# Kernel tuning notes

Hardware: AMD Instinct MI355X
Metric: run time of the kernel (lower is better)

Reference implementation:

```python
import jax, jax.numpy as jnp
import numpy as np

N_NODES = 50000
N_EDGES = 800000
DIM_IN = 64
DIM_H = 32
HEADS = 4
NUM_CLASSES = 10
NEG_SLOPE = 0.2  # DGL GATv2Conv default negative_slope


def _gatv2_layer(x, W_src, b_src, W_dst, b_dst, attn, src, dst):
    """DGL GATv2Conv (share_weights=False, eval mode so feat_drop is identity).
    x: [N, F_in]; attn: [H, D]; returns [N, H, D]."""
    N = x.shape[0]
    H, D = attn.shape
    fs = (x @ W_src + b_src).reshape(N, H, D)  # source projection
    fd = (x @ W_dst + b_dst).reshape(N, H, D)  # destination projection
    # per-edge additive attention: leaky_relu(fs[u] + fd[v]) . attn  -> [E, H]
    e = jax.nn.leaky_relu(fs[src] + fd[dst], NEG_SLOPE)  # [E, H, D]
    s = jnp.einsum('ehd,hd->eh', e, attn)  # [E, H]
    # edge softmax over incoming edges of each destination node
    smax = jax.lax.stop_gradient(
        jax.ops.segment_max(s, dst, num_segments=N))  # [N, H]
    es = jnp.exp(s - smax[dst])
    denom = jax.ops.segment_sum(es, dst, num_segments=N)  # [N, H]
    alpha = es / denom[dst]
    # weighted scatter-aggregate of source features
    out = jax.ops.segment_sum(alpha[:, :, None] * fs[src], dst, num_segments=N)
    return out  # [N, H, D]


def setup_inputs() -> dict:
    key = jax.random.key(0)
    ks = jax.random.split(key, 16)
    sc = 0.05
    inp = {
        'g_feats': jax.random.normal(ks[0], (N_NODES, DIM_IN), jnp.float32),
        'edge_src': jax.random.randint(ks[1], (N_EDGES,), 0, N_NODES, jnp.int32),
        'edge_dst': jax.random.randint(ks[2], (N_EDGES,), 0, N_NODES, jnp.int32),
        # input embedding Linear(dim_in, dim_h)
        'W_in': jax.random.normal(ks[3], (DIM_IN, DIM_H), jnp.float32) * sc,
        'b_in': jnp.zeros((DIM_H,), jnp.float32),
        # GATv2 layer 1: Linear(dim_h, heads*dim_h) for src/dst + attn [H, D]
        'W1_src': jax.random.normal(ks[4], (DIM_H, HEADS * DIM_H), jnp.float32) * sc,
        'b1_src': jnp.zeros((HEADS * DIM_H,), jnp.float32),
        'W1_dst': jax.random.normal(ks[5], (DIM_H, HEADS * DIM_H), jnp.float32) * sc,
        'b1_dst': jnp.zeros((HEADS * DIM_H,), jnp.float32),
        'attn1': jax.random.normal(ks[6], (HEADS, DIM_H), jnp.float32) * sc,
        # GATv2 layer 2
        'W2_src': jax.random.normal(ks[7], (DIM_H, HEADS * DIM_H), jnp.float32) * sc,
        'b2_src': jnp.zeros((HEADS * DIM_H,), jnp.float32),
        'W2_dst': jax.random.normal(ks[8], (DIM_H, HEADS * DIM_H), jnp.float32) * sc,
        'b2_dst': jnp.zeros((HEADS * DIM_H,), jnp.float32),
        'attn2': jax.random.normal(ks[9], (HEADS, DIM_H), jnp.float32) * sc,
        # MLP head: Linear(dim_h, dim_h) -> relu -> (dropout: eval) -> Linear(dim_h, num_classes)
        'Wh1': jax.random.normal(ks[10], (DIM_H, DIM_H), jnp.float32) * sc,
        'bh1': jnp.zeros((DIM_H,), jnp.float32),
        'Wh2': jax.random.normal(ks[11], (DIM_H, NUM_CLASSES), jnp.float32) * sc,
        'bh2': jnp.zeros((NUM_CLASSES,), jnp.float32),
    }
    return inp


def reference(g_feats, W_in, b_in,
              W1_src, b1_src, W1_dst, b1_dst, attn1,
              W2_src, b2_src, W2_dst, b2_dst, attn2,
              Wh1, bh1, Wh2, bh2,
              edge_src, edge_dst):
    x = g_feats @ W_in + b_in  # input embedding, [N, dim_h]
    h = _gatv2_layer(x, W1_src, b1_src, W1_dst, b1_dst, attn1, edge_src, edge_dst)
    h = jax.nn.relu(h.mean(axis=1))  # mean over heads -> [N, dim_h]
    h = _gatv2_layer(h, W2_src, b2_src, W2_dst, b2_dst, attn2, edge_src, edge_dst)
    h = h.mean(axis=1)  # [N, dim_h]
    # dgl.readout_nodes(op='mean') over the single graph -> [1, dim_h]
    g = h.mean(axis=0, keepdims=True)
    g = jax.nn.relu(g @ Wh1 + bh1)  # head (dropout inactive in eval)
    logits = g @ Wh2 + bh2
    return jax.nn.softmax(logits, axis=-1)  # [1, num_classes]
```

## Files before the change

### kernel.cpp

```cpp
#include <hip/hip_runtime.h>
#include <hip/hip_bf16.h>

#define N_NODES 50000
#define N_EDGES 800000
#define DIM_IN 64
#define DIM_H 32
#define HEADS 4
#define NCLS 10
#define NEG 0.2f
#define NBUCK 196
#define NPW 25
#define FSCALE 16.0f
#define LOG2E 1.44269504088896f

typedef float floatx2 __attribute__((ext_vector_type(2)));

__device__ __forceinline__ float fast_exp2(float x) {
#if __has_builtin(__builtin_amdgcn_exp2f)
    return __builtin_amdgcn_exp2f(x);
#else
    return __expf(x * 0.69314718055994531f);
#endif
}


__global__ void k_bhist(const int* __restrict__ dst, int* __restrict__ bh) {
    __shared__ int lh[NBUCK];
    for (int i = threadIdx.x; i < NBUCK; i += 256) lh[i] = 0;
    __syncthreads();
    int base = blockIdx.x * 1024 + threadIdx.x;
#pragma unroll
    for (int r = 0; r < 4; r++) {
        int e = base + r * 256;
        if (e < N_EDGES) atomicAdd(&lh[dst[e] >> 8], 1);
    }
    __syncthreads();
    for (int i = threadIdx.x; i < NBUCK; i += 256) {
        int c = lh[i];
        if (c) atomicAdd(&bh[i], c);
    }
}

__global__ void k_bscan(const int* __restrict__ bh, int* __restrict__ bbase,
                        int* __restrict__ gcur) {
    __shared__ int s[256];
    int t = threadIdx.x;
    int v = (t < NBUCK) ? bh[t] : 0;
    s[t] = v;
    __syncthreads();
    for (int off = 1; off < 256; off <<= 1) {
        int u = (t >= off) ? s[t - off] : 0;
        __syncthreads();
        s[t] += u;
        __syncthreads();
    }
    int excl = s[t] - v;
    if (t < NBUCK) {
        bbase[t] = excl;
        gcur[t] = excl;
    }
    if (t == 0) bbase[NBUCK] = N_EDGES;
}

__global__ void k_bin(const int* __restrict__ src, const int* __restrict__ dst,
                      int* __restrict__ gcur, unsigned* __restrict__ stage) {
    __shared__ int lh[NBUCK], chunk[NBUCK];
    int t = threadIdx.x;
    for (int i = t; i < NBUCK; i += 256) lh[i] = 0;
    __syncthreads();
    int e0 = blockIdx.x * 4096;
    unsigned pk[16];
    int bk[16];
#pragma unroll
    for (int r = 0; r < 16; r++) {
        int e = e0 + r * 256 + t;
        bool ok = e < N_EDGES;
        int s = ok ? src[e] : 0;
        int d = ok ? dst[e] : 0;
        bk[r] = ok ? (d >> 8) : -1;
        pk[r] = (unsigned)s | ((unsigned)(d & 255) << 16);
        if (ok) atomicAdd(&lh[bk[r]], 1);
    }
    __syncthreads();
    for (int i = t; i < NBUCK; i += 256) {
        int c = lh[i];
        chunk[i] = c ? atomicAdd(&gcur[i], c) : 0;
        lh[i] = 0;
    }
    __syncthreads();
#pragma unroll
    for (int r = 0; r < 16; r++) {
        if (bk[r] >= 0) {
            int lp = atomicAdd(&lh[bk[r]], 1);
            stage[chunk[bk[r]] + lp] = pk[r];
        }
    }
}

__global__ void k_csr(const unsigned* __restrict__ stage, const int* __restrict__ bbase,
                      int* __restrict__ row, unsigned short* __restrict__ adj) {
    __shared__ int lcnt[256], lcur[256], sc[256];
    int b = blockIdx.x, t = threadIdx.x;
    int s0 = bbase[b], s1 = bbase[b + 1];
    lcnt[t] = 0;
    __syncthreads();
    for (int i = s0 + t; i < s1; i += 256) atomicAdd(&lcnt[stage[i] >> 16], 1);
    __syncthreads();
    int v = lcnt[t];
    sc[t] = v;
    __syncthreads();
    for (int off = 1; off < 256; off <<= 1) {
        int u = (t >= off) ? sc[t - off] : 0;
        __syncthreads();
        sc[t] += u;
        __syncthreads();
    }
    int excl = sc[t] - v;
    int n = b * 256 + t;
    if (n < N_NODES) row[n] = s0 + excl;
    if (b == NBUCK - 1 && t == 0) row[N_NODES] = N_EDGES;
    lcur[t] = s0 + excl;
    __syncthreads();
    for (int i = s0 + t; i < s1; i += 256) {
        unsigned p = stage[i];
        int pos = atomicAdd(&lcur[p >> 16], 1);
        adj[pos] = (unsigned short)(p & 0xFFFFu);
    }
}


__device__ __forceinline__ unsigned short f2bf(float v) {
    unsigned u = __builtin_bit_cast(unsigned, v);
    u += 0x7FFFu + ((u >> 16) & 1u);
    return (unsigned short)(u >> 16);
}
__device__ __forceinline__ float bf2f(unsigned short h) {
    return __builtin_bit_cast(float, (unsigned)h << 16);
}

__global__ __launch_bounds__(256, 2) void k_fused1(
    const float* __restrict__ gf, const float* __restrict__ W_in,
    const float* __restrict__ b_in, const float* __restrict__ W1s,
    const float* __restrict__ b1s, const float* __restrict__ W1d,
    const float* __restrict__ b1d, unsigned char* __restrict__ fsh,
    unsigned short* __restrict__ fdh) {
    __shared__ float4 xb[4][2][8];
    int lane = threadIdx.x & 63;
    int wvl = threadIdx.x >> 6;
    int wave = (blockIdx.x * 256 + threadIdx.x) >> 6;
    int c = lane & 31, h = lane >> 5;
    int n0 = wave * NPW;
    if (n0 >= N_NODES) return;
    float wi[32];
#pragma unroll
    for (int k = 0; k < 32; k++) wi[k] = W_in[(h * 32 + k) * DIM_H + c];
    float bc = b_in[c];
    const float4* Wb = (lane < 32) ? (const float4*)W1s : (const float4*)W1d;
    const float4* bb = (lane < 32) ? (const float4*)b1s : (const float4*)b1d;
    float4 w[32];
#pragma unroll
    for (int k = 0; k < 32; k++) w[k] = Wb[k * 32 + c];
    float4 bias = bb[c];
#pragma unroll 2
    for (int i = 0; i < NPW; i++) {
        int nu = __builtin_amdgcn_readfirstlane(n0 + i);
        const float4* gr = (const float4*)(gf + (size_t)nu * DIM_IN + h * 32);
        float a1 = 0.f;
#pragma unroll
        for (int k4 = 0; k4 < 8; k4++) {
            float4 xv = gr[k4];
            a1 += xv.x * wi[k4 * 4 + 0];
            a1 += xv.y * wi[k4 * 4 + 1];
            a1 += xv.z * wi[k4 * 4 + 2];
            a1 += xv.w * wi[k4 * 4 + 3];
        }
        a1 += __shfl_xor(a1, 32, 64);
        if (lane < 32) ((float*)&xb[wvl][i & 1][0])[c] = a1 + bc;
        float4 acc = bias;
#pragma unroll
        for (int k4 = 0; k4 < 8; k4++) {
            float4 xv = xb[wvl][i & 1][k4];
#pragma unroll
            for (int j = 0; j < 4; j++) {
                float xk = (j == 0) ? xv.x : (j == 1) ? xv.y : (j == 2) ? xv.z : xv.w;
                float4 wk = w[k4 * 4 + j];
                acc.x += xk * wk.x;
                acc.y += xk * wk.y;
                acc.z += xk * wk.z;
                acc.w += xk * wk.w;
            }
        }
        if (lane < 32) {
            int pk = __builtin_amdgcn_cvt_pk_fp8_f32(acc.x * FSCALE, acc.y * FSCALE,
                                                     0, false);
            pk = __builtin_amdgcn_cvt_pk_fp8_f32(acc.z * FSCALE, acc.w * FSCALE,
                                                 pk, true);
            *(int*)&fsh[(size_t)nu * 128 + c * 4] = pk;
        } else {
            ushort4 o;
            o.x = f2bf(acc.x * FSCALE);
            o.y = f2bf(acc.y * FSCALE);
            o.z = f2bf(acc.z * FSCALE);
            o.w = f2bf(acc.w * FSCALE);
            *(ushort4*)&fdh[(size_t)nu * 128 + c * 4] = o;
        }
    }
}

__global__ __launch_bounds__(256, 2) void k_proj(
    const float* __restrict__ x, const float* __restrict__ Wsrc,
    const float* __restrict__ bsrc, const float* __restrict__ Wdst,
    const float* __restrict__ bdst, unsigned char* __restrict__ fsh,
    unsigned short* __restrict__ fdh) {
    int lane = threadIdx.x & 63;
    int wave = (blockIdx.x * 256 + threadIdx.x) >> 6;
    int cl = lane & 31;
    int n0 = wave * NPW;
    if (n0 >= N_NODES) return;
    const float4* Wb = (lane < 32) ? (const float4*)Wsrc : (const float4*)Wdst;
    const float4* bb = (lane < 32) ? (const float4*)bsrc : (const float4*)bdst;
    float4 w[32];
#pragma unroll
    for (int k = 0; k < 32; k++) w[k] = Wb[k * 32 + cl];
    float4 bias = bb[cl];
#pragma unroll 2
    for (int i = 0; i < NPW; i++) {
        int nu = __builtin_amdgcn_readfirstlane(n0 + i);
        const float4* xr = (const float4*)(x + (size_t)nu * DIM_H);
        float4 acc = bias;
#pragma unroll
        for (int k4 = 0; k4 < 8; k4++) {
            float4 xv = xr[k4];
#pragma unroll
            for (int j = 0; j < 4; j++) {
                float xk = (j == 0) ? xv.x : (j == 1) ? xv.y : (j == 2) ? xv.z : xv.w;
                float4 wk = w[k4 * 4 + j];
                acc.x += xk * wk.x;
                acc.y += xk * wk.y;
                acc.z += xk * wk.z;
                acc.w += xk * wk.w;
            }
        }
        if (lane < 32) {
            int pk = __builtin_amdgcn_cvt_pk_fp8_f32(acc.x * FSCALE, acc.y * FSCALE,
                                                     0, false);
            pk = __builtin_amdgcn_cvt_pk_fp8_f32(acc.z * FSCALE, acc.w * FSCALE,
                                                 pk, true);
            *(int*)&fsh[(size_t)nu * 128 + cl * 4] = pk;
        } else {
            ushort4 o;
            o.x = f2bf(acc.x * FSCALE);
            o.y = f2bf(acc.y * FSCALE);
            o.z = f2bf(acc.z * FSCALE);
            o.w = f2bf(acc.w * FSCALE);
            *(ushort4*)&fdh[(size_t)nu * 128 + cl * 4] = o;
        }
    }
}

__device__ __forceinline__ void pair_acc(unsigned u, floatx2 fd01, floatx2 fd23,
                                         floatx2 a01, floatx2 a23, floatx2& acc01,
                                         floatx2& acc23, float& den, bool valid) {
    floatx2 f01 = __builtin_amdgcn_cvt_pk_f32_fp8((int)u, false);
    floatx2 f23 = __builtin_amdgcn_cvt_pk_f32_fp8((int)u, true);
    floatx2 t01 = f01 + fd01;
    floatx2 t23 = f23 + fd23;
    floatx2 n01 = t01 * NEG;
    floatx2 n23 = t23 * NEG;
    floatx2 l01, l23;
    l01.x = fmaxf(t01.x, n01.x);
    l01.y = fmaxf(t01.y, n01.y);
    l23.x = fmaxf(t23.x, n23.x);
    l23.y = fmaxf(t23.y, n23.y);
    floatx2 d = l01 * a01 + l23 * a23;
    float p = d.x + d.y;
    p += __shfl_xor(p, 1, 64);
    p += __shfl_xor(p, 2, 64);
    p += __shfl_xor(p, 4, 64);
    float w = fast_exp2(p);
    if (!valid) w = 0.f;
    den += w;
    floatx2 wv = {w, w};
    acc01 += wv * f01;
    acc23 += wv * f23;
}

__global__ void k_gather(const unsigned char* __restrict__ fsh,
                         const unsigned short* __restrict__ fdh,
                         const float* __restrict__ attn, const int* __restrict__ row,
                         const unsigned short* __restrict__ adj,
                         float* __restrict__ xout, float* __restrict__ gpart,
                         int mode) {
    __shared__ float bsum[32];
    int tid = threadIdx.x;
    if (mode) {
        if (tid < 32) bsum[tid] = 0.f;
        __syncthreads();
    }
    int wave = tid >> 6;
    int lane = tid & 63;
    int n = blockIdx.x * 4 + wave;
    int sub = lane & 31, e2 = lane >> 5;
    unsigned suboff = (unsigned)sub << 2;
    float4 a4 = ((const float4*)attn)[sub];
    const float asc = LOG2E / FSCALE;
    floatx2 a01 = {a4.x * asc, a4.y * asc};
    floatx2 a23 = {a4.z * asc, a4.w * asc};
    ushort4 fdu = *(const ushort4*)(fdh + (size_t)n * 128 + sub * 4);
    floatx2 fd01 = {bf2f(fdu.x), bf2f(fdu.y)};
    floatx2 fd23 = {bf2f(fdu.z), bf2f(fdu.w)};
    floatx2 acc01 = {0.f, 0.f}, acc23 = {0.f, 0.f};
    float den = 0.f;
    int beg = row[n], end = row[n + 1];
    for (int base = beg; base < end; base += 64) {
        int m = end - base;
        if (m > 64) m = 64;
        int myadj = (lane < m) ? (int)adj[base + lane] : 0;
        int j = 0;
        for (; j + 16 <= m; j += 16) {
            unsigned o0 = ((unsigned)__shfl(myadj, j + 0 + e2, 64) << 7) + suboff;
            unsigned o1 = ((unsigned)__shfl(myadj, j + 2 + e2, 64) << 7) + suboff;
            unsigned o2 = ((unsigned)__shfl(myadj, j + 4 + e2, 64) << 7) + suboff;
            unsigned o3 = ((unsigned)__shfl(myadj, j + 6 + e2, 64) << 7) + suboff;
            unsigned o4 = ((unsigned)__shfl(myadj, j + 8 + e2, 64) << 7) + suboff;
            unsigned o5 = ((unsigned)__shfl(myadj, j + 10 + e2, 64) << 7) + suboff;
            unsigned o6 = ((unsigned)__shfl(myadj, j + 12 + e2, 64) << 7) + suboff;
            unsigned o7 = ((unsigned)__shfl(myadj, j + 14 + e2, 64) << 7) + suboff;
            unsigned u0 = *(const unsigned*)(fsh + o0);
            unsigned u1 = *(const unsigned*)(fsh + o1);
            unsigned u2 = *(const unsigned*)(fsh + o2);
            unsigned u3 = *(const unsigned*)(fsh + o3);
            unsigned u4 = *(const unsigned*)(fsh + o4);
            unsigned u5 = *(const unsigned*)(fsh + o5);
            unsigned u6 = *(const unsigned*)(fsh + o6);
            unsigned u7 = *(const unsigned*)(fsh + o7);
            pair_acc(u0, fd01, fd23, a01, a23, acc01, acc23, den, true);
            pair_acc(u1, fd01, fd23, a01, a23, acc01, acc23, den, true);
            pair_acc(u2, fd01, fd23, a01, a23, acc01, acc23, den, true);
            pair_acc(u3, fd01, fd23, a01, a23, acc01, acc23, den, true);
            pair_acc(u4, fd01, fd23, a01, a23, acc01, acc23, den, true);
            pair_acc(u5, fd01, fd23, a01, a23, acc01, acc23, den, true);
            pair_acc(u6, fd01, fd23, a01, a23, acc01, acc23, den, true);
            pair_acc(u7, fd01, fd23, a01, a23, acc01, acc23, den, true);
        }
        for (; j + 8 <= m; j += 8) {
            unsigned o0 = ((unsigned)__shfl(myadj, j + 0 + e2, 64) << 7) + suboff;
            unsigned o1 = ((unsigned)__shfl(myadj, j + 2 + e2, 64) << 7) + suboff;
            unsigned o2 = ((unsigned)__shfl(myadj, j + 4 + e2, 64) << 7) + suboff;
            unsigned o3 = ((unsigned)__shfl(myadj, j + 6 + e2, 64) << 7) + suboff;
            unsigned u0 = *(const unsigned*)(fsh + o0);
            unsigned u1 = *(const unsigned*)(fsh + o1);
            unsigned u2 = *(const unsigned*)(fsh + o2);
            unsigned u3 = *(const unsigned*)(fsh + o3);
            pair_acc(u0, fd01, fd23, a01, a23, acc01, acc23, den, true);
            pair_acc(u1, fd01, fd23, a01, a23, acc01, acc23, den, true);
            pair_acc(u2, fd01, fd23, a01, a23, acc01, acc23, den, true);
            pair_acc(u3, fd01, fd23, a01, a23, acc01, acc23, den, true);
        }
        for (; j < m; j += 2) {
            int idx = j + e2;
            bool valid = idx < m;
            unsigned o = ((unsigned)__shfl(myadj, valid ? idx : j, 64) << 7) + suboff;
            unsigned u = *(const unsigned*)(fsh + o);
            pair_acc(u, fd01, fd23, a01, a23, acc01, acc23, den, valid);
        }
    }
    den += __shfl_xor(den, 32, 64);
    float ax = acc01.x, ay = acc01.y, az = acc23.x, aw = acc23.y;
    ax += __shfl_xor(ax, 32, 64);
    ay += __shfl_xor(ay, 32, 64);
    az += __shfl_xor(az, 32, 64);
    aw += __shfl_xor(aw, 32, 64);
    float inv = den > 0.f ? (0.25f / FSCALE) / den : 0.f;
    float4 o;
    o.x = ax * inv;
    o.y = ay * inv;
    o.z = az * inv;
    o.w = aw * inv;
    o.x += __shfl_xor(o.x, 8, 64);
    o.y += __shfl_xor(o.y, 8, 64);
    o.z += __shfl_xor(o.z, 8, 64);
    o.w += __shfl_xor(o.w, 8, 64);
    o.x += __shfl_xor(o.x, 16, 64);
    o.y += __shfl_xor(o.y, 16, 64);
    o.z += __shfl_xor(o.z, 16, 64);
    o.w += __shfl_xor(o.w, 16, 64);
    if (mode == 0) {
        if (lane < 8) {
            o.x = fmaxf(o.x, 0.f);
            o.y = fmaxf(o.y, 0.f);
            o.z = fmaxf(o.z, 0.f);
            o.w = fmaxf(o.w, 0.f);
            ((float4*)(xout + (size_t)n * 32))[lane] = o;
        }
    } else {
        if (lane < 8) {
            atomicAdd(&bsum[lane * 4 + 0], o.x);
            atomicAdd(&bsum[lane * 4 + 1], o.y);
            atomicAdd(&bsum[lane * 4 + 2], o.z);
            atomicAdd(&bsum[lane * 4 + 3], o.w);
        }
        __syncthreads();
        if (tid < 32) atomicAdd(&gpart[(blockIdx.x & 63) * 32 + tid], bsum[tid]);
    }
}

__global__ void k_final(const float* __restrict__ gpart, const float* __restrict__ Wh1,
                        const float* __restrict__ bh1, const float* __restrict__ Wh2,
                        const float* __restrict__ bh2, float* __restrict__ out) {
    __shared__ float gv[32], gh[32], lg[16];
    int t = threadIdx.x;
    if (t < 32) {
        float s = 0.f;
        for (int b = 0; b < 64; b++) s += gpart[b * 32 + t];
        gv[t] = s * (1.f / (float)N_NODES);
    }
    __syncthreads();
    if (t < 32) {
        float s = bh1[t];
        for (int d = 0; d < 32; d++) s += gv[d] * Wh1[d * 32 + t];
        gh[t] = s > 0.f ? s : 0.f;
    }
    __syncthreads();
    if (t < NCLS) {
        float s = bh2[t];
        for (int j = 0; j < 32; j++) s += gh[j] * Wh2[j * NCLS + t];
        lg[t] = s;
    }
    __syncthreads();
    if (t == 0) {
        float m = lg[0];
        for (int c = 1; c < NCLS; c++) m = fmaxf(m, lg[c]);
        float ex[NCLS], sum = 0.f;
        for (int c = 0; c < NCLS; c++) {
            ex[c] = __expf(lg[c] - m);
            sum += ex[c];
        }
        float inv = 1.f / sum;
        for (int c = 0; c < NCLS; c++) out[c] = ex[c] * inv;
    }
}

extern "C" void kernel_launch(void* const* d_in, const int* in_sizes, int n_in,
                              void* d_out, int out_size, void* d_ws, size_t ws_size,
                              hipStream_t stream) {
    const float* g_feats = (const float*)d_in[0];
    const int* edge_src = (const int*)d_in[1];
    const int* edge_dst = (const int*)d_in[2];
    const float* W_in = (const float*)d_in[3];
    const float* b_in = (const float*)d_in[4];
    const float* W1_src = (const float*)d_in[5];
    const float* b1_src = (const float*)d_in[6];
    const float* W1_dst = (const float*)d_in[7];
    const float* b1_dst = (const float*)d_in[8];
    const float* attn1 = (const float*)d_in[9];
    const float* W2_src = (const float*)d_in[10];
    const float* b2_src = (const float*)d_in[11];
    const float* W2_dst = (const float*)d_in[12];
    const float* b2_dst = (const float*)d_in[13];
    const float* attn2 = (const float*)d_in[14];
    const float* Wh1 = (const float*)d_in[15];
    const float* bh1 = (const float*)d_in[16];
    const float* Wh2 = (const float*)d_in[17];
    const float* bh2 = (const float*)d_in[18];

    float* x = (float*)d_ws;
    unsigned char* fsh = (unsigned char*)(x + (size_t)N_NODES * 32);
    unsigned short* fdh = (unsigned short*)(fsh + (size_t)N_NODES * 128);
    float* gpart = (float*)(fdh + (size_t)N_NODES * 128);
    int* bh = (int*)(gpart + 64 * 32);
    int* bbase = bh + NBUCK;
    int* gcur = bbase + NBUCK + 1;
    int* row = gcur + NBUCK;
    unsigned* stage = (unsigned*)(row + N_NODES + 1);
    unsigned short* adj = (unsigned short*)(stage + N_EDGES);

    const int WB = (N_NODES / NPW + 3) / 4;

    hipMemsetAsync(gpart, 0, (64 * 32 + NBUCK) * sizeof(int), stream);

    k_bhist<<<(N_EDGES + 1023) / 1024, 256, 0, stream>>>(edge_dst, bh);
    k_bscan<<<1, 256, 0, stream>>>(bh, bbase, gcur);
    k_bin<<<(N_EDGES + 4095) / 4096, 256, 0, stream>>>(edge_src, edge_dst, gcur, stage);
    k_csr<<<NBUCK, 256, 0, stream>>>(stage, bbase, row, adj);

    k_fused1<<<WB, 256, 0, stream>>>(g_feats, W_in, b_in, W1_src, b1_src, W1_dst,
                                     b1_dst, fsh, fdh);
    k_gather<<<N_NODES / 4, 256, 0, stream>>>(fsh, fdh, attn1, row, adj, x, gpart, 0);

    k_proj<<<WB, 256, 0, stream>>>(x, W2_src, b2_src, W2_dst, b2_dst, fsh, fdh);
    k_gather<<<N_NODES / 4, 256, 0, stream>>>(fsh, fdh, attn2, row, adj, x, gpart, 1);

    k_final<<<1, 256, 0, stream>>>(gpart, Wh1, bh1, Wh2, bh2, (float*)d_out);
}
```

Measured before the change: 184.3 us.

## Merge histogram into projection kernel, batch gather nodes per wave with prefetch

```diff
diff --git a/kernel.cpp b/kernel.cpp
--- a/kernel.cpp
+++ b/kernel.cpp
@@ -12,6 +12,8 @@
 #define NPW 25
 #define FSCALE 16.0f
 #define LOG2E 1.44269504088896f
+#define NGRP 256
+#define NPG 8
 
 typedef float floatx2 __attribute__((ext_vector_type(2)));
 
@@ -23,23 +25,6 @@
 #endif
 }
 
-
-__global__ void k_bhist(const int* __restrict__ dst, int* __restrict__ bh) {
-    __shared__ int lh[NBUCK];
-    for (int i = threadIdx.x; i < NBUCK; i += 256) lh[i] = 0;
-    __syncthreads();
-    int base = blockIdx.x * 1024 + threadIdx.x;
-#pragma unroll
-    for (int r = 0; r < 4; r++) {
-        int e = base + r * 256;
-        if (e < N_EDGES) atomicAdd(&lh[dst[e] >> 8], 1);
-    }
-    __syncthreads();
-    for (int i = threadIdx.x; i < NBUCK; i += 256) {
-        int c = lh[i];
-        if (c) atomicAdd(&bh[i], c);
-    }
-}
 
 __global__ void k_bscan(const int* __restrict__ bh, int* __restrict__ bbase,
                         int* __restrict__ gcur) {
@@ -138,28 +123,51 @@
     return __builtin_bit_cast(float, (unsigned)h << 16);
 }
 
-__global__ __launch_bounds__(256, 2) void k_fused1(
+#define F1B 500
+#define HB 782
+__global__ __launch_bounds__(256, 2) void k_f1h(
     const float* __restrict__ gf, const float* __restrict__ W_in,
     const float* __restrict__ b_in, const float* __restrict__ W1s,
     const float* __restrict__ b1s, const float* __restrict__ W1d,
     const float* __restrict__ b1d, unsigned char* __restrict__ fsh,
-    unsigned short* __restrict__ fdh) {
+    unsigned short* __restrict__ fdh, const int* __restrict__ dst,
+    int* __restrict__ bhist) {
     __shared__ float4 xb[4][2][8];
+    __shared__ int lh[NBUCK];
+    if (blockIdx.x >= F1B) {
+        for (int i = threadIdx.x; i < NBUCK; i += 256) lh[i] = 0;
+        __syncthreads();
+        int base = (blockIdx.x - F1B) * 1024 + threadIdx.x;
+#pragma unroll
+        for (int r = 0; r < 4; r++) {
+            int e = base + r * 256;
+            if (e < N_EDGES) atomicAdd(&lh[dst[e] >> 8], 1);
+        }
+        __syncthreads();
+        for (int i = threadIdx.x; i < NBUCK; i += 256) {
+            int c = lh[i];
+            if (c) atomicAdd(&bhist[i], c);
+        }
+        return;
+    }
     int lane = threadIdx.x & 63;
     int wvl = threadIdx.x >> 6;
     int wave = (blockIdx.x * 256 + threadIdx.x) >> 6;
     int c = lane & 31, h = lane >> 5;
     int n0 = wave * NPW;
-    if (n0 >= N_NODES) return;
     float wi[32];
 #pragma unroll
     for (int k = 0; k < 32; k++) wi[k] = W_in[(h * 32 + k) * DIM_H + c];
     float bc = b_in[c];
     const float4* Wb = (lane < 32) ? (const float4*)W1s : (const float4*)W1d;
     const float4* bb = (lane < 32) ? (const float4*)b1s : (const float4*)b1d;
-    float4 w[32];
-#pragma unroll
-    for (int k = 0; k < 32; k++) w[k] = Wb[k * 32 + c];
+    floatx2 wA[32], wB[32];
+#pragma unroll
+    for (int k = 0; k < 32; k++) {
+        float4 wf = Wb[k * 32 + c];
+        wA[k] = {wf.x, wf.y};
+        wB[k] = {wf.z, wf.w};
+    }
     float4 bias = bb[c];
 #pragma unroll 2
     for (int i = 0; i < NPW; i++) {
@@ -176,32 +184,30 @@
         }
         a1 += __shfl_xor(a1, 32, 64);
         if (lane < 32) ((float*)&xb[wvl][i & 1][0])[c] = a1 + bc;
-        float4 acc = bias;
+        floatx2 acc01 = {bias.x, bias.y}, acc23 = {bias.z, bias.w};
 #pragma unroll
         for (int k4 = 0; k4 < 8; k4++) {
             float4 xv = xb[wvl][i & 1][k4];
 #pragma unroll
             for (int j = 0; j < 4; j++) {
                 float xk = (j == 0) ? xv.x : (j == 1) ? xv.y : (j == 2) ? xv.z : xv.w;
-                float4 wk = w[k4 * 4 + j];
-                acc.x += xk * wk.x;
-                acc.y += xk * wk.y;
-                acc.z += xk * wk.z;
-                acc.w += xk * wk.w;
+                floatx2 xx = {xk, xk};
+                acc01 += xx * wA[k4 * 4 + j];
+                acc23 += xx * wB[k4 * 4 + j];
             }
         }
         if (lane < 32) {
-            int pk = __builtin_amdgcn_cvt_pk_fp8_f32(acc.x * FSCALE, acc.y * FSCALE,
+            int pk = __builtin_amdgcn_cvt_pk_fp8_f32(acc01.x * FSCALE, acc01.y * FSCALE,
                                                      0, false);
-            pk = __builtin_amdgcn_cvt_pk_fp8_f32(acc.z * FSCALE, acc.w * FSCALE,
+            pk = __builtin_amdgcn_cvt_pk_fp8_f32(acc23.x * FSCALE, acc23.y * FSCALE,
                                                  pk, true);
             *(int*)&fsh[(size_t)nu * 128 + c * 4] = pk;
         } else {
             ushort4 o;
-            o.x = f2bf(acc.x * FSCALE);
-            o.y = f2bf(acc.y * FSCALE);
-            o.z = f2bf(acc.z * FSCALE);
-            o.w = f2bf(acc.w * FSCALE);
+            o.x = f2bf(acc01.x * FSCALE);
+            o.y = f2bf(acc01.y * FSCALE);
+            o.z = f2bf(acc23.x * FSCALE);
+            o.w = f2bf(acc23.y * FSCALE);
             *(ushort4*)&fdh[(size_t)nu * 128 + c * 4] = o;
         }
     }
@@ -219,40 +225,42 @@
     if (n0 >= N_NODES) return;
     const float4* Wb = (lane < 32) ? (const float4*)Wsrc : (const float4*)Wdst;
     const float4* bb = (lane < 32) ? (const float4*)bsrc : (const float4*)bdst;
-    float4 w[32];
-#pragma unroll
-    for (int k = 0; k < 32; k++) w[k] = Wb[k * 32 + cl];
+    floatx2 wA[32], wB[32];
+#pragma unroll
+    for (int k = 0; k < 32; k++) {
+        float4 wf = Wb[k * 32 + cl];
+        wA[k] = {wf.x, wf.y};
+        wB[k] = {wf.z, wf.w};
+    }
     float4 bias = bb[cl];
 #pragma unroll 2
     for (int i = 0; i < NPW; i++) {
         int nu = __builtin_amdgcn_readfirstlane(n0 + i);
         const float4* xr = (const float4*)(x + (size_t)nu * DIM_H);
-        float4 acc = bias;
+        floatx2 acc01 = {bias.x, bias.y}, acc23 = {bias.z, bias.w};
 #pragma unroll
         for (int k4 = 0; k4 < 8; k4++) {
             float4 xv = xr[k4];
 #pragma unroll
             for (int j = 0; j < 4; j++) {
                 float xk = (j == 0) ? xv.x : (j == 1) ? xv.y : (j == 2) ? xv.z : xv.w;
-                float4 wk = w[k4 * 4 + j];
-                acc.x += xk * wk.x;
-                acc.y += xk * wk.y;
-                acc.z += xk * wk.z;
-                acc.w += xk * wk.w;
+                floatx2 xx = {xk, xk};
+                acc01 += xx * wA[k4 * 4 + j];
+                acc23 += xx * wB[k4 * 4 + j];
             }
         }
         if (lane < 32) {
-            int pk = __builtin_amdgcn_cvt_pk_fp8_f32(acc.x * FSCALE, acc.y * FSCALE,
+            int pk = __builtin_amdgcn_cvt_pk_fp8_f32(acc01.x * FSCALE, acc01.y * FSCALE,
                                                      0, false);
-            pk = __builtin_amdgcn_cvt_pk_fp8_f32(acc.z * FSCALE, acc.w * FSCALE,
+            pk = __builtin_amdgcn_cvt_pk_fp8_f32(acc23.x * FSCALE, acc23.y * FSCALE,
                                                  pk, true);
             *(int*)&fsh[(size_t)nu * 128 + cl * 4] = pk;
         } else {
             ushort4 o;
-            o.x = f2bf(acc.x * FSCALE);
-            o.y = f2bf(acc.y * FSCALE);
-            o.z = f2bf(acc.z * FSCALE);
-            o.w = f2bf(acc.w * FSCALE);
+            o.x = f2bf(acc01.x * FSCALE);
+            o.y = f2bf(acc01.y * FSCALE);
+            o.z = f2bf(acc23.x * FSCALE);
+            o.w = f2bf(acc23.y * FSCALE);
             *(ushort4*)&fdh[(size_t)nu * 128 + cl * 4] = o;
         }
     }
@@ -285,123 +293,155 @@
     acc23 += wv * f23;
 }
 
-__global__ void k_gather(const unsigned char* __restrict__ fsh,
-                         const unsigned short* __restrict__ fdh,
-                         const float* __restrict__ attn, const int* __restrict__ row,
-                         const unsigned short* __restrict__ adj,
-                         float* __restrict__ xout, float* __restrict__ gpart,
-                         int mode) {
-    __shared__ float bsum[32];
-    int tid = threadIdx.x;
-    if (mode) {
-        if (tid < 32) bsum[tid] = 0.f;
-        __syncthreads();
-    }
-    int wave = tid >> 6;
-    int lane = tid & 63;
-    int n = blockIdx.x * 4 + wave;
+__global__ __launch_bounds__(256) void k_gather(
+    const unsigned char* __restrict__ fsh, const unsigned short* __restrict__ fdh,
+    const float* __restrict__ attn, const int* __restrict__ row,
+    const unsigned short* __restrict__ adj, float* __restrict__ xout,
+    float* __restrict__ gpart, int mode) {
+    int lane = threadIdx.x & 63;
+    int wg = (blockIdx.x * 256 + threadIdx.x) >> 6;
+    int nb = wg * NPG;
+    if (nb >= N_NODES) return;
     int sub = lane & 31, e2 = lane >> 5;
     unsigned suboff = (unsigned)sub << 2;
+    const float asc = LOG2E / FSCALE;
     float4 a4 = ((const float4*)attn)[sub];
-    const float asc = LOG2E / FSCALE;
     floatx2 a01 = {a4.x * asc, a4.y * asc};
     floatx2 a23 = {a4.z * asc, a4.w * asc};
-    ushort4 fdu = *(const ushort4*)(fdh + (size_t)n * 128 + sub * 4);
-    floatx2 fd01 = {bf2f(fdu.x), bf2f(fdu.y)};
-    floatx2 fd23 = {bf2f(fdu.z), bf2f(fdu.w)};
-    floatx2 acc01 = {0.f, 0.f}, acc23 = {0.f, 0.f};
-    float den = 0.f;
-    int beg = row[n], end = row[n + 1];
-    for (int base = beg; base < end; base += 64) {
-        int m = end - base;
-        if (m > 64) m = 64;
-        int myadj = (lane < m) ? (int)adj[base + lane] : 0;
-        int j = 0;
-        for (; j + 16 <= m; j += 16) {
-            unsigned o0 = ((unsigned)__shfl(myadj, j + 0 + e2, 64) << 7) + suboff;
-            unsigned o1 = ((unsigned)__shfl(myadj, j + 2 + e2, 64) << 7) + suboff;
-            unsigned o2 = ((unsigned)__shfl(myadj, j + 4 + e2, 64) << 7) + suboff;
-            unsigned o3 = ((unsigned)__shfl(myadj, j + 6 + e2, 64) << 7) + suboff;
-            unsigned o4 = ((unsigned)__shfl(myadj, j + 8 + e2, 64) << 7) + suboff;
-            unsigned o5 = ((unsigned)__shfl(myadj, j + 10 + e2, 64) << 7) + suboff;
-            unsigned o6 = ((unsigned)__shfl(myadj, j + 12 + e2, 64) << 7) + suboff;
-            unsigned o7 = ((unsigned)__shfl(myadj, j + 14 + e2, 64) << 7) + suboff;
-            unsigned u0 = *(const unsigned*)(fsh + o0);
-            unsigned u1 = *(const unsigned*)(fsh + o1);
-            unsigned u2 = *(const unsigned*)(fsh + o2);
-            unsigned u3 = *(const unsigned*)(fsh + o3);
-            unsigned u4 = *(const unsigned*)(fsh + o4);
-            unsigned u5 = *(const unsigned*)(fsh + o5);
-            unsigned u6 = *(const unsigned*)(fsh + o6);
-            unsigned u7 = *(const unsigned*)(fsh + o7);
-            pair_acc(u0, fd01, fd23, a01, a23, acc01, acc23, den, true);
-            pair_acc(u1, fd01, fd23, a01, a23, acc01, acc23, den, true);
-            pair_acc(u2, fd01, fd23, a01, a23, acc01, acc23, den, true);
-            pair_acc(u3, fd01, fd23, a01, a23, acc01, acc23, den, true);
-            pair_acc(u4, fd01, fd23, a01, a23, acc01, acc23, den, true);
-            pair_acc(u5, fd01, fd23, a01, a23, acc01, acc23, den, true);
-            pair_acc(u6, fd01, fd23, a01, a23, acc01, acc23, den, true);
-            pair_acc(u7, fd01, fd23, a01, a23, acc01, acc23, den, true);
-        }
-        for (; j + 8 <= m; j += 8) {
-            unsigned o0 = ((unsigned)__shfl(myadj, j + 0 + e2, 64) << 7) + suboff;
-            unsigned o1 = ((unsigned)__shfl(myadj, j + 2 + e2, 64) << 7) + suboff;
-            unsigned o2 = ((unsigned)__shfl(myadj, j + 4 + e2, 64) << 7) + suboff;
-            unsigned o3 = ((unsigned)__shfl(myadj, j + 6 + e2, 64) << 7) + suboff;
-            unsigned u0 = *(const unsigned*)(fsh + o0);
-            unsigned u1 = *(const unsigned*)(fsh + o1);
-            unsigned u2 = *(const unsigned*)(fsh + o2);
-            unsigned u3 = *(const unsigned*)(fsh + o3);
-            pair_acc(u0, fd01, fd23, a01, a23, acc01, acc23, den, true);
-            pair_acc(u1, fd01, fd23, a01, a23, acc01, acc23, den, true);
-            pair_acc(u2, fd01, fd23, a01, a23, acc01, acc23, den, true);
-            pair_acc(u3, fd01, fd23, a01, a23, acc01, acc23, den, true);
-        }
-        for (; j < m; j += 2) {
-            int idx = j + e2;
-            bool valid = idx < m;
-            unsigned o = ((unsigned)__shfl(myadj, valid ? idx : j, 64) << 7) + suboff;
-            unsigned u = *(const unsigned*)(fsh + o);
-            pair_acc(u, fd01, fd23, a01, a23, acc01, acc23, den, valid);
-        }
-    }
-    den += __shfl_xor(den, 32, 64);
-    float ax = acc01.x, ay = acc01.y, az = acc23.x, aw = acc23.y;
-    ax += __shfl_xor(ax, 32, 64);
-    ay += __shfl_xor(ay, 32, 64);
-    az += __shfl_xor(az, 32, 64);
-    aw += __shfl_xor(aw, 32, 64);
-    float inv = den > 0.f ? (0.25f / FSCALE) / den : 0.f;
-    float4 o;
-    o.x = ax * inv;
-    o.y = ay * inv;
-    o.z = az * inv;
-    o.w = aw * inv;
-    o.x += __shfl_xor(o.x, 8, 64);
-    o.y += __shfl_xor(o.y, 8, 64);
-    o.z += __shfl_xor(o.z, 8, 64);
-    o.w += __shfl_xor(o.w, 8, 64);
-    o.x += __shfl_xor(o.x, 16, 64);
-    o.y += __shfl_xor(o.y, 16, 64);
-    o.z += __shfl_xor(o.z, 16, 64);
-    o.w += __shfl_xor(o.w, 16, 64);
-    if (mode == 0) {
-        if (lane < 8) {
-            o.x = fmaxf(o.x, 0.f);
-            o.y = fmaxf(o.y, 0.f);
-            o.z = fmaxf(o.z, 0.f);
-            o.w = fmaxf(o.w, 0.f);
-            ((float4*)(xout + (size_t)n * 32))[lane] = o;
-        }
-    } else {
-        if (lane < 8) {
-            atomicAdd(&bsum[lane * 4 + 0], o.x);
-            atomicAdd(&bsum[lane * 4 + 1], o.y);
-            atomicAdd(&bsum[lane * 4 + 2], o.z);
-            atomicAdd(&bsum[lane * 4 + 3], o.w);
-        }
-        __syncthreads();
-        if (tid < 32) atomicAdd(&gpart[(blockIdx.x & 63) * 32 + tid], bsum[tid]);
+    int rv = (lane < NPG + 1) ? row[nb + lane] : 0;
+    ushort4 fdu = *(const ushort4*)(fdh + (size_t)nb * 128 + sub * 4);
+    int beg = __shfl(rv, 0, 64), end = __shfl(rv, 1, 64);
+    {
+        int m0 = end - beg;
+        if (m0 > 64) m0 = 64;
+        int a0 = (lane < m0) ? (int)adj[beg + lane] : 0;
+        rv = rv;
+        (void)a0;
+    }
+    int m0i = end - beg;
+    if (m0i > 64) m0i = 64;
+    int adjc = (lane < m0i) ? (int)adj[beg + lane] : 0;
+    float4 racc = {0.f, 0.f, 0.f, 0.f};
+#pragma unroll 1
+    for (int i = 0; i < NPG; i++) {
+        int n = nb + i;
+        ushort4 fdu_n = fdu;
+        int adjc_n = 0, beg_n = 0, end_n = 0;
+        if (i < NPG - 1) {
+            beg_n = __shfl(rv, i + 1, 64);
+            end_n = __shfl(rv, i + 2, 64);
+            fdu_n = *(const ushort4*)(fdh + (size_t)(n + 1) * 128 + sub * 4);
+            int mn = end_n - beg_n;
+            if (mn > 64) mn = 64;
+            adjc_n = (lane < mn) ? (int)adj[beg_n + lane] : 0;
+        }
+        floatx2 fd01 = {bf2f(fdu.x), bf2f(fdu.y)};
+        floatx2 fd23 = {bf2f(fdu.z), bf2f(fdu.w)};
+        floatx2 acc01 = {0.f, 0.f}, acc23 = {0.f, 0.f};
+        float den = 0.f;
+        for (int base = beg; base < end; base += 64) {
+            int m = end - base;
+            if (m > 64) m = 64;
+            int myadj;
+            if (base == beg) {
+                myadj = adjc;
+            } else {
+                myadj = (lane < m) ? (int)adj[base + lane] : 0;
+            }
+            int j = 0;
+            for (; j + 16 <= m; j += 16) {
+                unsigned o0 = ((unsigned)__shfl(myadj, j + 0 + e2, 64) << 7) + suboff;
+                unsigned o1 = ((unsigned)__shfl(myadj, j + 2 + e2, 64) << 7) + suboff;
+                unsigned o2 = ((unsigned)__shfl(myadj, j + 4 + e2, 64) << 7) + suboff;
+                unsigned o3 = ((unsigned)__shfl(myadj, j + 6 + e2, 64) << 7) + suboff;
+                unsigned o4 = ((unsigned)__shfl(myadj, j + 8 + e2, 64) << 7) + suboff;
+                unsigned o5 = ((unsigned)__shfl(myadj, j + 10 + e2, 64) << 7) + suboff;
+                unsigned o6 = ((unsigned)__shfl(myadj, j + 12 + e2, 64) << 7) + suboff;
+                unsigned o7 = ((unsigned)__shfl(myadj, j + 14 + e2, 64) << 7) + suboff;
+                unsigned u0 = *(const unsigned*)(fsh + o0);
+                unsigned u1 = *(const unsigned*)(fsh + o1);
+                unsigned u2 = *(const unsigned*)(fsh + o2);
+                unsigned u3 = *(const unsigned*)(fsh + o3);
+                unsigned u4 = *(const unsigned*)(fsh + o4);
+                unsigned u5 = *(const unsigned*)(fsh + o5);
+                unsigned u6 = *(const unsigned*)(fsh + o6);
+                unsigned u7 = *(const unsigned*)(fsh + o7);
+                pair_acc(u0, fd01, fd23, a01, a23, acc01, acc23, den, true);
+                pair_acc(u1, fd01, fd23, a01, a23, acc01, acc23, den, true);
+                pair_acc(u2, fd01, fd23, a01, a23, acc01, acc23, den, true);
+                pair_acc(u3, fd01, fd23, a01, a23, acc01, acc23, den, true);
+                pair_acc(u4, fd01, fd23, a01, a23, acc01, acc23, den, true);
+                pair_acc(u5, fd01, fd23, a01, a23, acc01, acc23, den, true);
+                pair_acc(u6, fd01, fd23, a01, a23, acc01, acc23, den, true);
+                pair_acc(u7, fd01, fd23, a01, a23, acc01, acc23, den, true);
+            }
+            for (; j + 8 <= m; j += 8) {
+                unsigned o0 = ((unsigned)__shfl(myadj, j + 0 + e2, 64) << 7) + suboff;
+                unsigned o1 = ((unsigned)__shfl(myadj, j + 2 + e2, 64) << 7) + suboff;
+                unsigned o2 = ((unsigned)__shfl(myadj, j + 4 + e2, 64) << 7) + suboff;
+                unsigned o3 = ((unsigned)__shfl(myadj, j + 6 + e2, 64) << 7) + suboff;
+                unsigned u0 = *(const unsigned*)(fsh + o0);
+                unsigned u1 = *(const unsigned*)(fsh + o1);
+                unsigned u2 = *(const unsigned*)(fsh + o2);
+                unsigned u3 = *(const unsigned*)(fsh + o3);
+                pair_acc(u0, fd01, fd23, a01, a23, acc01, acc23, den, true);
+                pair_acc(u1, fd01, fd23, a01, a23, acc01, acc23, den, true);
+                pair_acc(u2, fd01, fd23, a01, a23, acc01, acc23, den, true);
+                pair_acc(u3, fd01, fd23, a01, a23, acc01, acc23, den, true);
+            }
+            for (; j < m; j += 2) {
+                int idx = j + e2;
+                bool valid = idx < m;
+                unsigned o = ((unsigned)__shfl(myadj, valid ? idx : j, 64) << 7) + suboff;
+                unsigned u = *(const unsigned*)(fsh + o);
+                pair_acc(u, fd01, fd23, a01, a23, acc01, acc23, den, valid);
+            }
+        }
+        den += __shfl_xor(den, 32, 64);
+        float ax = acc01.x, ay = acc01.y, az = acc23.x, aw = acc23.y;
+        ax += __shfl_xor(ax, 32, 64);
+        ay += __shfl_xor(ay, 32, 64);
+        az += __shfl_xor(az, 32, 64);
+        aw += __shfl_xor(aw, 32, 64);
+        float inv = den > 0.f ? (0.25f / FSCALE) / den : 0.f;
+        float4 o;
+        o.x = ax * inv;
+        o.y = ay * inv;
+        o.z = az * inv;
+        o.w = aw * inv;
+        o.x += __shfl_xor(o.x, 8, 64);
+        o.y += __shfl_xor(o.y, 8, 64);
+        o.z += __shfl_xor(o.z, 8, 64);
+        o.w += __shfl_xor(o.w, 8, 64);
+        o.x += __shfl_xor(o.x, 16, 64);
+        o.y += __shfl_xor(o.y, 16, 64);
+        o.z += __shfl_xor(o.z, 16, 64);
+        o.w += __shfl_xor(o.w, 16, 64);
+        if (mode == 0) {
+            if (lane < 8) {
+                o.x = fmaxf(o.x, 0.f);
+                o.y = fmaxf(o.y, 0.f);
+                o.z = fmaxf(o.z, 0.f);
+                o.w = fmaxf(o.w, 0.f);
+                ((float4*)(xout + (size_t)n * 32))[lane] = o;
+            }
+        } else {
+            racc.x += o.x;
+            racc.y += o.y;
+            racc.z += o.z;
+            racc.w += o.w;
+        }
+        fdu = fdu_n;
+        adjc = adjc_n;
+        beg = beg_n;
+        end = end_n;
+    }
+    if (mode == 1 && lane < 8) {
+        float* gp = gpart + (wg & (NGRP - 1)) * 32 + lane * 4;
+        atomicAdd(&gp[0], racc.x);
+        atomicAdd(&gp[1], racc.y);
+        atomicAdd(&gp[2], racc.z);
+        atomicAdd(&gp[3], racc.w);
     }
 }
 
@@ -412,7 +452,7 @@
     int t = threadIdx.x;
     if (t < 32) {
         float s = 0.f;
-        for (int b = 0; b < 64; b++) s += gpart[b * 32 + t];
+        for (int b = 0; b < NGRP; b++) s += gpart[b * 32 + t];
         gv[t] = s * (1.f / (float)N_NODES);
     }
     __syncthreads();
@@ -468,28 +508,29 @@
     unsigned char* fsh = (unsigned char*)(x + (size_t)N_NODES * 32);
     unsigned short* fdh = (unsigned short*)(fsh + (size_t)N_NODES * 128);
     float* gpart = (float*)(fdh + (size_t)N_NODES * 128);
-    int* bh = (int*)(gpart + 64 * 32);
-    int* bbase = bh + NBUCK;
+    int* bhist = (int*)(gpart + NGRP * 32);
+    int* bbase = bhist + NBUCK;
     int* gcur = bbase + NBUCK + 1;
     int* row = gcur + NBUCK;
     unsigned* stage = (unsigned*)(row + N_NODES + 1);
     unsigned short* adj = (unsigned short*)(stage + N_EDGES);
 
-    const int WB = (N_NODES / NPW + 3) / 4;
-
-    hipMemsetAsync(gpart, 0, (64 * 32 + NBUCK) * sizeof(int), stream);
-
-    k_bhist<<<(N_EDGES + 1023) / 1024, 256, 0, stream>>>(edge_dst, bh);
-    k_bscan<<<1, 256, 0, stream>>>(bh, bbase, gcur);
+    const int PB = (N_NODES / NPW + 3) / 4;
+    const int GB = (N_NODES / NPG + 3) / 4;
+
+    hipMemsetAsync(gpart, 0, (NGRP * 32 + NBUCK) * sizeof(int), stream);
+
+    k_f1h<<<F1B + HB, 256, 0, stream>>>(g_feats, W_in, b_in, W1_src, b1_src, W1_dst,
+                                        b1_dst, fsh, fdh, edge_dst, bhist);
+
+    k_bscan<<<1, 256, 0, stream>>>(bhist, bbase, gcur);
     k_bin<<<(N_EDGES + 4095) / 4096, 256, 0, stream>>>(edge_src, edge_dst, gcur, stage);
     k_csr<<<NBUCK, 256, 0, stream>>>(stage, bbase, row, adj);
 
-    k_fused1<<<WB, 256, 0, stream>>>(g_feats, W_in, b_in, W1_src, b1_src, W1_dst,
-                                     b1_dst, fsh, fdh);
-    k_gather<<<N_NODES / 4, 256, 0, stream>>>(fsh, fdh, attn1, row, adj, x, gpart, 0);
-
-    k_proj<<<WB, 256, 0, stream>>>(x, W2_src, b2_src, W2_dst, b2_dst, fsh, fdh);
-    k_gather<<<N_NODES / 4, 256, 0, stream>>>(fsh, fdh, attn2, row, adj, x, gpart, 1);
+    k_gather<<<GB, 256, 0, stream>>>(fsh, fdh, attn1, row, adj, x, gpart, 0);
+
+    k_proj<<<PB, 256, 0, stream>>>(x, W2_src, b2_src, W2_dst, b2_dst, fsh, fdh);
+    k_gather<<<GB, 256, 0, stream>>>(fsh, fdh, attn2, row, adj, x, gpart, 1);
 
     k_final<<<1, 256, 0, stream>>>(gpart, Wh1, bh1, Wh2, bh2, (float*)d_out);
 }
```

New measurement: 188.4 us. 2.2% more time.
